# Kernel optimization log

Hardware: AMD Instinct MI355X
Metric: run time of the kernel (lower is better)

## Reference

```python
import jax, jax.numpy as jnp
import numpy as np


def setup_inputs() -> dict:
    key = jax.random.key(0)
    ks = jax.random.split(key, 8)
    B, C, H, W = 16, 512, 96, 96
    Cr = C // 8
    s = 0.02
    return {
        "x": jax.random.normal(ks[0], (B, C, H, W), jnp.float32),
        "Wq": jax.random.normal(ks[1], (Cr, C), jnp.float32) * s,
        "bq": jax.random.normal(ks[2], (Cr,), jnp.float32) * s,
        "Wk": jax.random.normal(ks[3], (Cr, C), jnp.float32) * s,
        "bk": jax.random.normal(ks[4], (Cr,), jnp.float32) * s,
        "Wv": jax.random.normal(ks[5], (C, C), jnp.float32) * s,
        "bv": jax.random.normal(ks[6], (C,), jnp.float32) * s,
        "gamma": jax.random.normal(ks[7], (1,), jnp.float32) * 0.1,
    }


def _conv1x1(x, W, b):
    # 1x1 conv == channel contraction: [B,C,H,W] x [O,C] -> [B,O,H,W]
    return jnp.einsum('bchw,oc->bohw', x, W) + b[None, :, None, None]


def reference(x, Wq, bq, Wk, bk, Wv, bv, gamma):
    B, C, H, W = x.shape
    q = _conv1x1(x, Wq, bq)   # [B,Cr,H,W]
    k = _conv1x1(x, Wk, bk)   # [B,Cr,H,W]
    v = _conv1x1(x, Wv, bv)   # [B,C,H,W]

    # energy along column (vertical): query at (i,w), keys at (j,w) -> [B,H,W,H]
    eh = jnp.einsum('bciw,bcjw->biwj', q, k)
    # energy along row (horizontal): query at (h,i), keys at (h,j) -> [B,H,W,W]
    ew = jnp.einsum('bchi,bchj->bhij', q, k)

    attn = jax.nn.softmax(jnp.concatenate([eh, ew], axis=-1), axis=-1)  # [B,H,W,H+W]
    ah = attn[..., :H]   # [B,H,W,H]
    aw = attn[..., H:]   # [B,H,W,W]

    out_h = jnp.einsum('bcjw,biwj->bciw', v, ah)  # vertical aggregation
    out_w = jnp.einsum('bchj,bhij->bchi', v, aw)  # horizontal aggregation
    out = out_h + out_w
    return gamma[0] * out + x
```

## Files before the change

kernel.cpp:

```cpp
#include <hip/hip_runtime.h>
#include <hip/hip_bf16.h>

#define DI __device__ __forceinline__

typedef short bf16x8 __attribute__((ext_vector_type(8)));
typedef float f32x4 __attribute__((ext_vector_type(4)));
typedef unsigned short u16;
typedef u16 u16x2 __attribute__((ext_vector_type(2)));
typedef u16 u16x8 __attribute__((ext_vector_type(8)));

#define B_ 16
#define C_ 512
#define CR_ 64
#define H_ 96
#define HW_ 9216
#define K_ 512

DI float b2f(u16 u){ unsigned v = ((unsigned)u)<<16; float f; __builtin_memcpy(&f,&v,4); return f; }
DI u16 f2b(float f){ unsigned v; __builtin_memcpy(&v,&f,4); v += 0x7fff + ((v>>16)&1); return (u16)(v>>16); }

DI void gload16(const void* g, void* l){
  __builtin_amdgcn_global_load_lds((const __attribute__((address_space(1))) unsigned*)g,
                                   (__attribute__((address_space(3))) unsigned*)l, 16, 0, 0);
}

__global__ __launch_bounds__(256) void k_pack(const float* __restrict__ Wq, const float* __restrict__ bq,
    const float* __restrict__ Wk, const float* __restrict__ bk,
    const float* __restrict__ Wv, const float* __restrict__ bv,
    u16* __restrict__ Wcat, float* __restrict__ bcat){
  int gid = blockIdx.x*256 + threadIdx.x;
  int o = gid >> 9, c = gid & 511;
  float w = (o < 64) ? Wq[o*512 + c] : (o < 128) ? Wk[(o-64)*512 + c] : Wv[(o-128)*512 + c];
  Wcat[gid] = f2b(w);
  if (c == 0) bcat[o] = (o < 64) ? bq[o] : (o < 128) ? bk[o-64] : bv[o-128];
}

__global__ __launch_bounds__(256) void k_xt(const float* __restrict__ x, u16* __restrict__ xt){
  int bx = blockIdx.x;
  int pt = bx % 144; int ct = (bx/144) & 7; int b = bx / (144*8);
  __shared__ u16 tile[64][68];
  int tx = threadIdx.x & 63, ty = threadIdx.x >> 6;
  const float* xb = x + (size_t)b*C_*HW_;
  for (int r = ty; r < 64; r += 4)
    tile[r][tx] = f2b(xb[(size_t)(ct*64 + r)*HW_ + pt*64 + tx]);
  __syncthreads();
  u16* xtb = xt + (size_t)b*HW_*K_;
  for (int r = ty; r < 64; r += 4)
    xtb[(size_t)(pt*64 + r)*K_ + ct*64 + tx] = tile[tx][r];
}

__global__ __launch_bounds__(256) void k_qkv(const u16* __restrict__ Wcat, const float* __restrict__ bcat,
    const u16* __restrict__ xt, u16* __restrict__ q, u16* __restrict__ k, u16* __restrict__ v){
  int bx = blockIdx.x;
  int wg = (bx & 7)*720 + (bx >> 3);
  int nt = wg % 72; int tmp = wg / 72; int mt = tmp % 5; int b = tmp / 5;
  __shared__ u16 As[128*64];
  __shared__ u16 Bs[128*64];
  int lane = threadIdx.x & 63, wid = threadIdx.x >> 6;
  int wr = wid >> 1, wc = wid & 1;
  const u16* xb = xt + (size_t)b*HW_*K_ + (size_t)nt*128*K_;
  const u16* Ab = Wcat + (size_t)mt*128*K_;

  f32x4 acc[4][4];
  #pragma unroll
  for (int i=0;i<4;++i)
    #pragma unroll
    for (int j=0;j<4;++j) acc[i][j] = (f32x4){0.f,0.f,0.f,0.f};

  int ibase = wid*4;
  for (int kt=0; kt<8; ++kt){
    int k0 = kt*64;
    __syncthreads();
    #pragma unroll
    for (int i=0;i<4;++i){
      int byteL = ((ibase + i)<<10) + (lane<<4);
      int row = byteL >> 7;
      int slog = ((byteL >> 4) & 7) ^ (row & 7);
      size_t ge = (size_t)row*K_ + (k0 + slog*8);
      gload16(Ab + ge, (char*)As + ((ibase+i)<<10));
      gload16(xb + ge, (char*)Bs + ((ibase+i)<<10));
    }
    __syncthreads();
    bf16x8 af[4][2], bfr[4][2];
    #pragma unroll
    for (int f=0; f<4; ++f){
      #pragma unroll
      for (int kk=0; kk<2; ++kk){
        int sl = kk*4 + (lane >> 4);
        int ra = wr*64 + f*16 + (lane & 15);
        af[f][kk]  = *(const bf16x8*)((const char*)As + ra*128 + ((sl ^ (ra & 7))<<4));
        int rb = wc*64 + f*16 + (lane & 15);
        bfr[f][kk] = *(const bf16x8*)((const char*)Bs + rb*128 + ((sl ^ (rb & 7))<<4));
      }
    }
    #pragma unroll
    for (int fm=0; fm<4; ++fm)
      #pragma unroll
      for (int fn=0; fn<4; ++fn)
        #pragma unroll
        for (int kk=0; kk<2; ++kk)
          acc[fm][fn] = __builtin_amdgcn_mfma_f32_16x16x32_bf16(af[fm][kk], bfr[fn][kk], acc[fm][fn], 0, 0, 0);
  }
  int r4 = lane >> 4, cl = lane & 15;
  for (int fm=0; fm<4; ++fm){
    for (int j=0;j<4;++j){
      int o = mt*128 + wr*64 + fm*16 + r4*4 + j;
      float bias = bcat[o];
      for (int fn=0; fn<4; ++fn){
        int n = nt*128 + wc*64 + fn*16 + cl;
        u16 bv16 = f2b(acc[fm][fn][j] + bias);
        if (o < 64)       q[((size_t)b*CR_ + o)*HW_ + n] = bv16;
        else if (o < 128) k[((size_t)b*CR_ + (o-64))*HW_ + n] = bv16;
        else              v[((size_t)b*C_ + (o-128))*HW_ + n] = bv16;
      }
    }
  }
}

__global__ __launch_bounds__(256) void k_tr(const u16* __restrict__ q, const u16* __restrict__ k,
    const u16* __restrict__ v, u16* __restrict__ qt, u16* __restrict__ kt, u16* __restrict__ vt){
  int bx = blockIdx.x;
  int ch = bx % 640; int b = bx / 640;
  const u16* src; u16* dst;
  if (ch < 64)      { src = q + ((size_t)b*CR_ + ch)*HW_;      dst = qt + ((size_t)b*CR_ + ch)*HW_; }
  else if (ch < 128){ src = k + ((size_t)b*CR_ + ch-64)*HW_;   dst = kt + ((size_t)b*CR_ + ch-64)*HW_; }
  else              { src = v + ((size_t)b*C_ + ch-128)*HW_;   dst = vt + ((size_t)b*C_ + ch-128)*HW_; }
  __shared__ u16 t[96][100];
  for (int e = threadIdx.x; e < HW_; e += 256) t[e/96][e%96] = src[e];
  __syncthreads();
  for (int e = threadIdx.x; e < HW_; e += 256) dst[e] = t[e%96][e/96];
}

__global__ __launch_bounds__(256) void k_scores(const u16* __restrict__ q, const u16* __restrict__ k,
    const u16* __restrict__ qt, const u16* __restrict__ kt, u16* __restrict__ att){
  int bx = blockIdx.x;
  int p = bx % 96; int b = (bx/96) & 15; int mode = bx / 1536;
  __shared__ float Qs[64*96];
  __shared__ float Ks[64*96];
  const u16* qsrc; const u16* ksrc;
  if (mode == 0){ qsrc = qt + (size_t)b*CR_*HW_ + p*96; ksrc = kt + (size_t)b*CR_*HW_ + p*96; }
  else          { qsrc = q  + (size_t)b*CR_*HW_ + p*96; ksrc = k  + (size_t)b*CR_*HW_ + p*96; }
  for (int u = threadIdx.x; u < 64*12; u += 256){
    int c = u / 12, ch = u % 12;
    u16x8 a = *(const u16x8*)(qsrc + (size_t)c*HW_ + ch*8);
    u16x8 d = *(const u16x8*)(ksrc + (size_t)c*HW_ + ch*8);
    #pragma unroll
    for (int e=0;e<8;++e){ Qs[c*96 + ch*8 + e] = b2f(a[e]); Ks[c*96 + ch*8 + e] = b2f(d[e]); }
  }
  __syncthreads();
  int ti = threadIdx.x >> 4, tj = threadIdx.x & 15;
  float acc[6][6];
  #pragma unroll
  for (int a2=0;a2<6;++a2)
    #pragma unroll
    for (int b2=0;b2<6;++b2) acc[a2][b2] = 0.f;
  for (int c=0;c<64;++c){
    float qv[6], kv[6];
    #pragma unroll
    for (int a2=0;a2<6;++a2){ qv[a2] = Qs[c*96 + ti + 16*a2]; kv[a2] = Ks[c*96 + tj + 16*a2]; }
    #pragma unroll
    for (int a2=0;a2<6;++a2)
      #pragma unroll
      for (int b2=0;b2<6;++b2) acc[a2][b2] += qv[a2]*kv[b2];
  }
  for (int a2=0;a2<6;++a2){
    int i = ti + 16*a2;
    for (int b2=0;b2<6;++b2){
      int j = tj + 16*b2;
      size_t idx = (mode==0) ? ((size_t)((b*96 + i)*96 + p))*192 + j
                             : ((size_t)((b*96 + p)*96 + i))*192 + 96 + j;
      att[idx] = f2b(acc[a2][b2]);
    }
  }
}

__global__ __launch_bounds__(256) void k_softmax(u16* __restrict__ att){
  int row = blockIdx.x*4 + (threadIdx.x >> 6);
  int lane = threadIdx.x & 63;
  u16* r = att + (size_t)row*192;
  float s0 = b2f(r[lane]), s1 = b2f(r[lane+64]), s2 = b2f(r[lane+128]);
  float m = fmaxf(fmaxf(s0,s1),s2);
  #pragma unroll
  for (int off=32; off; off>>=1) m = fmaxf(m, __shfl_xor(m, off));
  float e0 = expf(s0-m), e1 = expf(s1-m), e2 = expf(s2-m);
  float s = e0+e1+e2;
  #pragma unroll
  for (int off=32; off; off>>=1) s += __shfl_xor(s, off);
  float inv = 1.0f/s;
  r[lane] = f2b(e0*inv); r[lane+64] = f2b(e1*inv); r[lane+128] = f2b(e2*inv);
}

__global__ __launch_bounds__(512) void k_outh(const u16* __restrict__ vt, const u16* __restrict__ att,
    u16* __restrict__ oh){
  int bx = blockIdx.x; int w = bx % 96, b = bx / 96;
  __shared__ u16 Ah[96*104];
  for (int u = threadIdx.x; u < 96*48; u += 512){
    int i = u/48, jc = u%48;
    *(u16x2*)&Ah[i*104 + jc*2] = *(const u16x2*)(att + ((size_t)((b*96 + i)*96 + w))*192 + jc*2);
  }
  __syncthreads();
  int lane = threadIdx.x & 63, wid = threadIdx.x >> 6;
  int cl = lane & 15, r4 = lane >> 4;
  f32x4 acc[4][6];
  #pragma unroll
  for (int i=0;i<4;++i)
    #pragma unroll
    for (int j=0;j<6;++j) acc[i][j] = (f32x4){0.f,0.f,0.f,0.f};
  const u16* vb = vt + (size_t)b*C_*HW_ + (size_t)w*96;
  #pragma unroll
  for (int kt=0; kt<3; ++kt){
    int kof = kt*32 + r4*8;
    bf16x8 a[4], bb[6];
    #pragma unroll
    for (int fm=0; fm<4; ++fm){
      int c = wid*64 + fm*16 + cl;
      a[fm] = *(const bf16x8*)(vb + (size_t)c*HW_ + kof);
    }
    #pragma unroll
    for (int fn=0; fn<6; ++fn)
      bb[fn] = *(const bf16x8*)&Ah[(fn*16 + cl)*104 + kof];
    #pragma unroll
    for (int fm=0; fm<4; ++fm)
      #pragma unroll
      for (int fn=0; fn<6; ++fn)
        acc[fm][fn] = __builtin_amdgcn_mfma_f32_16x16x32_bf16(a[fm], bb[fn], acc[fm][fn], 0, 0, 0);
  }
  u16* ob = oh + ((size_t)(b*96 + w))*C_*96;
  for (int fm=0; fm<4; ++fm)
    for (int fn=0; fn<6; ++fn)
      for (int j=0;j<4;++j){
        int c = wid*64 + fm*16 + r4*4 + j;
        int i = fn*16 + cl;
        ob[(size_t)c*96 + i] = f2b(acc[fm][fn][j]);
      }
}

__global__ __launch_bounds__(512) void k_outw(const u16* __restrict__ v, const u16* __restrict__ att,
    const float* __restrict__ gp, float* __restrict__ out){
  int bx = blockIdx.x; int h = bx % 96, b = bx / 96;
  __shared__ u16 Aw[96*104];
  for (int u = threadIdx.x; u < 96*48; u += 512){
    int i = u/48, jc = u%48;
    *(u16x2*)&Aw[i*104 + jc*2] = *(const u16x2*)(att + ((size_t)((b*96 + h)*96 + i))*192 + 96 + jc*2);
  }
  __syncthreads();
  float g = gp[0];
  int lane = threadIdx.x & 63, wid = threadIdx.x >> 6;
  int cl = lane & 15, r4 = lane >> 4;
  f32x4 acc[4][6];
  #pragma unroll
  for (int i=0;i<4;++i)
    #pragma unroll
    for (int j=0;j<6;++j) acc[i][j] = (f32x4){0.f,0.f,0.f,0.f};
  const u16* vb = v + (size_t)b*C_*HW_ + (size_t)h*96;
  #pragma unroll
  for (int kt=0; kt<3; ++kt){
    int kof = kt*32 + r4*8;
    bf16x8 a[4], bb[6];
    #pragma unroll
    for (int fm=0; fm<4; ++fm){
      int c = wid*64 + fm*16 + cl;
      a[fm] = *(const bf16x8*)(vb + (size_t)c*HW_ + kof);
    }
    #pragma unroll
    for (int fn=0; fn<6; ++fn)
      bb[fn] = *(const bf16x8*)&Aw[(fn*16 + cl)*104 + kof];
    #pragma unroll
    for (int fm=0; fm<4; ++fm)
      #pragma unroll
      for (int fn=0; fn<6; ++fn)
        acc[fm][fn] = __builtin_amdgcn_mfma_f32_16x16x32_bf16(a[fm], bb[fn], acc[fm][fn], 0, 0, 0);
  }
  float* ob = out + (size_t)b*C_*HW_ + (size_t)h*96;
  for (int fm=0; fm<4; ++fm)
    for (int fn=0; fn<6; ++fn)
      for (int j=0;j<4;++j){
        int c = wid*64 + fm*16 + r4*4 + j;
        int i = fn*16 + cl;
        ob[(size_t)c*HW_ + i] = g * acc[fm][fn][j];
      }
}

__global__ __launch_bounds__(256) void k_final(const u16* __restrict__ oh, const float* __restrict__ x,
    const float* __restrict__ gp, float* __restrict__ out){
  int bx = blockIdx.x; int c = bx & 511; int b = bx >> 9;
  __shared__ u16 T[96*104];
  const u16* ohb = oh + (size_t)(b*96)*C_*96 + (size_t)c*96;
  for (int e = threadIdx.x; e < HW_; e += 256){
    int w = e/96, i = e%96;
    T[w*104 + i] = ohb[(size_t)w*C_*96 + i];
  }
  __syncthreads();
  float g = gp[0];
  size_t base = ((size_t)b*C_ + c)*HW_;
  for (int e = threadIdx.x; e < HW_; e += 256){
    int i = e/96, w = e%96;
    out[base + e] = out[base + e] + g*b2f(T[w*104 + i]) + x[base + e];
  }
}

extern "C" void kernel_launch(void* const* d_in, const int* in_sizes, int n_in,
                              void* d_out, int out_size, void* d_ws, size_t ws_size,
                              hipStream_t stream) {
  (void)in_sizes; (void)n_in; (void)out_size; (void)ws_size;
  const float* x  = (const float*)d_in[0];
  const float* Wq = (const float*)d_in[1];
  const float* bq = (const float*)d_in[2];
  const float* Wk = (const float*)d_in[3];
  const float* bk = (const float*)d_in[4];
  const float* Wv = (const float*)d_in[5];
  const float* bv = (const float*)d_in[6];
  const float* gm = (const float*)d_in[7];
  float* out = (float*)d_out;
  char* ws = (char*)d_ws;

  u16*  Wcat = (u16*)(ws);
  float* bcat= (float*)(ws + 655360);
  u16*  q    = (u16*)(ws + 659456);
  u16*  k    = (u16*)(ws + 19533824);
  u16*  qt   = (u16*)(ws + 38408192);
  u16*  kt   = (u16*)(ws + 57282560);
  u16*  v    = (u16*)(ws + 76156928);
  u16*  att  = (u16*)(ws + 227151872);
  u16*  oh   = (u16*)(ws + 283774976);
  u16*  xt   = (u16*)d_out;
  u16*  vt   = xt + 75497472ull;

  k_pack   <<<1280, 256, 0, stream>>>(Wq,bq,Wk,bk,Wv,bv,Wcat,bcat);
  k_xt     <<<18432,256, 0, stream>>>(x, xt);
  k_qkv    <<<5760, 256, 0, stream>>>(Wcat,bcat,xt,q,k,v);
  k_tr     <<<10240,256, 0, stream>>>(q,k,v,qt,kt,vt);
  k_scores <<<3072, 256, 0, stream>>>(q,k,qt,kt,att);
  k_softmax<<<36864,256, 0, stream>>>(att);
  k_outh   <<<1536, 512, 0, stream>>>(vt,att,oh);
  k_outw   <<<1536, 512, 0, stream>>>(v,att,gm,out);
  k_final  <<<8192, 256, 0, stream>>>(oh,x,gm,out);
}
```

Before: 890.5 us.

## Vectorize transposes, write bf16 outputs in place, and fuse final epilogue

Rewrites the x and q/k/v transposes to use 16-byte vector loads and stores through XOR-swizzled shared memory. Softmax now handles rows with 32 lanes and fast exp. The two aggregation kernels write bf16 results in place over their V inputs, replacing the fp32 out write and the separate oh buffer. The final kernel then reads both bf16 partials with vector accesses and applies gamma and the residual. This reduces global traffic, especially the fp32 read-modify-write of out, at the cost of bf16 rounding of the horizontal partial and in-place overwrites that depend on each block reading its full V slice before writing.

Result: faster. 824.6 us (-7.4%).

```diff
diff --git a/kernel.cpp b/kernel.cpp
--- a/kernel.cpp
+++ b/kernel.cpp
@@ -7,6 +7,7 @@
 typedef float f32x4 __attribute__((ext_vector_type(4)));
 typedef unsigned short u16;
 typedef u16 u16x2 __attribute__((ext_vector_type(2)));
+typedef u16 u16x4 __attribute__((ext_vector_type(4)));
 typedef u16 u16x8 __attribute__((ext_vector_type(8)));
 
 #define B_ 16
@@ -38,15 +39,23 @@
 __global__ __launch_bounds__(256) void k_xt(const float* __restrict__ x, u16* __restrict__ xt){
   int bx = blockIdx.x;
   int pt = bx % 144; int ct = (bx/144) & 7; int b = bx / (144*8);
-  __shared__ u16 tile[64][68];
-  int tx = threadIdx.x & 63, ty = threadIdx.x >> 6;
-  const float* xb = x + (size_t)b*C_*HW_;
-  for (int r = ty; r < 64; r += 4)
-    tile[r][tx] = f2b(xb[(size_t)(ct*64 + r)*HW_ + pt*64 + tx]);
-  __syncthreads();
-  u16* xtb = xt + (size_t)b*HW_*K_;
-  for (int r = ty; r < 64; r += 4)
-    xtb[(size_t)(pt*64 + r)*K_ + ct*64 + tx] = tile[tx][r];
+  __shared__ u16 T[64*72];
+  const float* xb = x + (size_t)b*C_*HW_ + (size_t)(ct*64)*HW_ + pt*64;
+  for (int it = threadIdx.x; it < 1024; it += 256){
+    int r = it & 63, px4 = it >> 6;
+    f32x4 f4 = *(const f32x4*)(xb + (size_t)r*HW_ + px4*4);
+    #pragma unroll
+    for (int e=0;e<4;++e) T[(px4*4 + e)*72 + r] = f2b(f4[e]);
+  }
+  __syncthreads();
+  u16* xtb = xt + (size_t)b*HW_*K_ + (size_t)(pt*64)*K_ + ct*64;
+  for (int it = threadIdx.x; it < 512; it += 256){
+    int c8 = it & 7, p = it >> 3;
+    u16x8 o;
+    #pragma unroll
+    for (int e=0;e<8;++e) o[e] = T[p*72 + c8*8 + e];
+    *(u16x8*)(xtb + (size_t)p*K_ + c8*8) = o;
+  }
 }
 
 __global__ __launch_bounds__(256) void k_qkv(const u16* __restrict__ Wcat, const float* __restrict__ bcat,
@@ -117,18 +126,32 @@
   }
 }
 
-__global__ __launch_bounds__(256) void k_tr(const u16* __restrict__ q, const u16* __restrict__ k,
+__global__ __launch_bounds__(256) void k_tr(const u16* __restrict__ q, const u16* __restrict__ kk,
     const u16* __restrict__ v, u16* __restrict__ qt, u16* __restrict__ kt, u16* __restrict__ vt){
   int bx = blockIdx.x;
   int ch = bx % 640; int b = bx / 640;
   const u16* src; u16* dst;
-  if (ch < 64)      { src = q + ((size_t)b*CR_ + ch)*HW_;      dst = qt + ((size_t)b*CR_ + ch)*HW_; }
-  else if (ch < 128){ src = k + ((size_t)b*CR_ + ch-64)*HW_;   dst = kt + ((size_t)b*CR_ + ch-64)*HW_; }
-  else              { src = v + ((size_t)b*C_ + ch-128)*HW_;   dst = vt + ((size_t)b*C_ + ch-128)*HW_; }
-  __shared__ u16 t[96][100];
-  for (int e = threadIdx.x; e < HW_; e += 256) t[e/96][e%96] = src[e];
-  __syncthreads();
-  for (int e = threadIdx.x; e < HW_; e += 256) dst[e] = t[e%96][e/96];
+  if (ch < 64)      { src = q  + ((size_t)b*CR_ + ch)*HW_;     dst = qt + ((size_t)b*CR_ + ch)*HW_; }
+  else if (ch < 128){ src = kk + ((size_t)b*CR_ + ch-64)*HW_;  dst = kt + ((size_t)b*CR_ + ch-64)*HW_; }
+  else              { src = v  + ((size_t)b*C_ + ch-128)*HW_;  dst = vt + ((size_t)b*C_ + ch-128)*HW_; }
+  __shared__ u16 T[96*128];
+  for (int it = threadIdx.x; it < 1152; it += 256){
+    int h = it / 12, c8 = it % 12;
+    u16x8 v8 = *(const u16x8*)(src + h*96 + c8*8);
+    int sp = (h >> 3) ^ (c8 & 7);
+    #pragma unroll
+    for (int e = 0; e < 8; ++e){
+      int w = c8*8 + e;
+      T[w*128 + sp*8 + (h & 7)] = v8[e];
+    }
+  }
+  __syncthreads();
+  for (int it = threadIdx.x; it < 1152; it += 256){
+    int w = it / 12, h8 = it % 12;
+    int sp = h8 ^ ((w >> 3) & 7);
+    u16x8 o = *(const u16x8*)&T[w*128 + sp*8];
+    *(u16x8*)(dst + (size_t)w*96 + h8*8) = o;
+  }
 }
 
 __global__ __launch_bounds__(256) void k_scores(const u16* __restrict__ q, const u16* __restrict__ k,
@@ -175,23 +198,24 @@
 }
 
 __global__ __launch_bounds__(256) void k_softmax(u16* __restrict__ att){
-  int row = blockIdx.x*4 + (threadIdx.x >> 6);
-  int lane = threadIdx.x & 63;
-  u16* r = att + (size_t)row*192;
-  float s0 = b2f(r[lane]), s1 = b2f(r[lane+64]), s2 = b2f(r[lane+128]);
-  float m = fmaxf(fmaxf(s0,s1),s2);
-  #pragma unroll
-  for (int off=32; off; off>>=1) m = fmaxf(m, __shfl_xor(m, off));
-  float e0 = expf(s0-m), e1 = expf(s1-m), e2 = expf(s2-m);
-  float s = e0+e1+e2;
-  #pragma unroll
-  for (int off=32; off; off>>=1) s += __shfl_xor(s, off);
+  int row = blockIdx.x*8 + (threadIdx.x >> 5);
+  int sub = threadIdx.x & 31;
+  u16* r = att + (size_t)row*192 + sub*6;
+  u16x2 a = *(u16x2*)r, b = *(u16x2*)(r+2), c = *(u16x2*)(r+4);
+  float v0=b2f(a[0]),v1=b2f(a[1]),v2=b2f(b[0]),v3=b2f(b[1]),v4=b2f(c[0]),v5=b2f(c[1]);
+  float m = fmaxf(fmaxf(fmaxf(v0,v1),fmaxf(v2,v3)),fmaxf(v4,v5));
+  #pragma unroll
+  for (int off=16; off; off>>=1) m = fmaxf(m, __shfl_xor(m, off));
+  float e0=__expf(v0-m),e1=__expf(v1-m),e2=__expf(v2-m),e3=__expf(v3-m),e4=__expf(v4-m),e5=__expf(v5-m);
+  float s = ((e0+e1)+(e2+e3))+(e4+e5);
+  #pragma unroll
+  for (int off=16; off; off>>=1) s += __shfl_xor(s, off);
   float inv = 1.0f/s;
-  r[lane] = f2b(e0*inv); r[lane+64] = f2b(e1*inv); r[lane+128] = f2b(e2*inv);
-}
-
-__global__ __launch_bounds__(512) void k_outh(const u16* __restrict__ vt, const u16* __restrict__ att,
-    u16* __restrict__ oh){
+  a[0]=f2b(e0*inv); a[1]=f2b(e1*inv); b[0]=f2b(e2*inv); b[1]=f2b(e3*inv); c[0]=f2b(e4*inv); c[1]=f2b(e5*inv);
+  *(u16x2*)r = a; *(u16x2*)(r+2) = b; *(u16x2*)(r+4) = c;
+}
+
+__global__ __launch_bounds__(512) void k_outh(u16* vo, const u16* __restrict__ att){
   int bx = blockIdx.x; int w = bx % 96, b = bx / 96;
   __shared__ u16 Ah[96*104];
   for (int u = threadIdx.x; u < 96*48; u += 512){
@@ -206,7 +230,7 @@
   for (int i=0;i<4;++i)
     #pragma unroll
     for (int j=0;j<6;++j) acc[i][j] = (f32x4){0.f,0.f,0.f,0.f};
-  const u16* vb = vt + (size_t)b*C_*HW_ + (size_t)w*96;
+  u16* vb = vo + (size_t)b*C_*HW_ + (size_t)w*96;
   #pragma unroll
   for (int kt=0; kt<3; ++kt){
     int kof = kt*32 + r4*8;
@@ -225,18 +249,16 @@
       for (int fn=0; fn<6; ++fn)
         acc[fm][fn] = __builtin_amdgcn_mfma_f32_16x16x32_bf16(a[fm], bb[fn], acc[fm][fn], 0, 0, 0);
   }
-  u16* ob = oh + ((size_t)(b*96 + w))*C_*96;
   for (int fm=0; fm<4; ++fm)
     for (int fn=0; fn<6; ++fn)
       for (int j=0;j<4;++j){
         int c = wid*64 + fm*16 + r4*4 + j;
         int i = fn*16 + cl;
-        ob[(size_t)c*96 + i] = f2b(acc[fm][fn][j]);
+        vb[(size_t)c*HW_ + i] = f2b(acc[fm][fn][j]);
       }
 }
 
-__global__ __launch_bounds__(512) void k_outw(const u16* __restrict__ v, const u16* __restrict__ att,
-    const float* __restrict__ gp, float* __restrict__ out){
+__global__ __launch_bounds__(512) void k_outw(u16* vo, const u16* __restrict__ att){
   int bx = blockIdx.x; int h = bx % 96, b = bx / 96;
   __shared__ u16 Aw[96*104];
   for (int u = threadIdx.x; u < 96*48; u += 512){
@@ -244,7 +266,6 @@
     *(u16x2*)&Aw[i*104 + jc*2] = *(const u16x2*)(att + ((size_t)((b*96 + h)*96 + i))*192 + 96 + jc*2);
   }
   __syncthreads();
-  float g = gp[0];
   int lane = threadIdx.x & 63, wid = threadIdx.x >> 6;
   int cl = lane & 15, r4 = lane >> 4;
   f32x4 acc[4][6];
@@ -252,7 +273,7 @@
   for (int i=0;i<4;++i)
     #pragma unroll
     for (int j=0;j<6;++j) acc[i][j] = (f32x4){0.f,0.f,0.f,0.f};
-  const u16* vb = v + (size_t)b*C_*HW_ + (size_t)h*96;
+  u16* vb = vo + (size_t)b*C_*HW_ + (size_t)h*96;
   #pragma unroll
   for (int kt=0; kt<3; ++kt){
     int kof = kt*32 + r4*8;
@@ -271,31 +292,44 @@
       for (int fn=0; fn<6; ++fn)
         acc[fm][fn] = __builtin_amdgcn_mfma_f32_16x16x32_bf16(a[fm], bb[fn], acc[fm][fn], 0, 0, 0);
   }
-  float* ob = out + (size_t)b*C_*HW_ + (size_t)h*96;
   for (int fm=0; fm<4; ++fm)
     for (int fn=0; fn<6; ++fn)
       for (int j=0;j<4;++j){
         int c = wid*64 + fm*16 + r4*4 + j;
         int i = fn*16 + cl;
-        ob[(size_t)c*HW_ + i] = g * acc[fm][fn][j];
+        vb[(size_t)c*HW_ + i] = f2b(acc[fm][fn][j]);
       }
 }
 
-__global__ __launch_bounds__(256) void k_final(const u16* __restrict__ oh, const float* __restrict__ x,
-    const float* __restrict__ gp, float* __restrict__ out){
+__global__ __launch_bounds__(256) void k_final(const u16* oh, const u16* ow,
+    const float* __restrict__ x, const float* __restrict__ gp, float* __restrict__ out){
   int bx = blockIdx.x; int c = bx & 511; int b = bx >> 9;
-  __shared__ u16 T[96*104];
-  const u16* ohb = oh + (size_t)(b*96)*C_*96 + (size_t)c*96;
-  for (int e = threadIdx.x; e < HW_; e += 256){
-    int w = e/96, i = e%96;
-    T[w*104 + i] = ohb[(size_t)w*C_*96 + i];
+  size_t base = ((size_t)b*C_ + c)*HW_;
+  const u16* ohc = oh + base;
+  const u16* owc = ow + base;
+  __shared__ u16 T[96*128];
+  for (int it = threadIdx.x; it < 1152; it += 256){
+    int w = it / 12, c8 = it % 12;
+    u16x8 v8 = *(const u16x8*)(ohc + w*96 + c8*8);
+    int sp = (w >> 3) ^ (c8 & 7);
+    #pragma unroll
+    for (int e = 0; e < 8; ++e){
+      int i = c8*8 + e;
+      T[i*128 + sp*8 + (w & 7)] = v8[e];
+    }
   }
   __syncthreads();
   float g = gp[0];
-  size_t base = ((size_t)b*C_ + c)*HW_;
-  for (int e = threadIdx.x; e < HW_; e += 256){
-    int i = e/96, w = e%96;
-    out[base + e] = out[base + e] + g*b2f(T[w*104 + i]) + x[base + e];
+  for (int it = threadIdx.x; it < 2304; it += 256){
+    int i = it / 24, w4 = it % 24; int w = w4*4;
+    int sp = (w >> 3) ^ ((i >> 3) & 7);
+    u16x4 t4 = *(const u16x4*)&T[i*128 + sp*8 + (w & 7)];
+    u16x4 o4 = *(const u16x4*)(owc + i*96 + w);
+    f32x4 x4 = *(const f32x4*)(x + base + i*96 + w);
+    f32x4 r;
+    #pragma unroll
+    for (int e=0;e<4;++e) r[e] = g*(b2f(t4[e]) + b2f(o4[e])) + x4[e];
+    *(f32x4*)(out + base + i*96 + w) = r;
   }
 }
 
@@ -322,17 +356,16 @@
   u16*  kt   = (u16*)(ws + 57282560);
   u16*  v    = (u16*)(ws + 76156928);
   u16*  att  = (u16*)(ws + 227151872);
-  u16*  oh   = (u16*)(ws + 283774976);
+  u16*  vt   = (u16*)(ws + 283774976);
   u16*  xt   = (u16*)d_out;
-  u16*  vt   = xt + 75497472ull;
 
   k_pack   <<<1280, 256, 0, stream>>>(Wq,bq,Wk,bk,Wv,bv,Wcat,bcat);
   k_xt     <<<18432,256, 0, stream>>>(x, xt);
   k_qkv    <<<5760, 256, 0, stream>>>(Wcat,bcat,xt,q,k,v);
   k_tr     <<<10240,256, 0, stream>>>(q,k,v,qt,kt,vt);
   k_scores <<<3072, 256, 0, stream>>>(q,k,qt,kt,att);
-  k_softmax<<<36864,256, 0, stream>>>(att);
-  k_outh   <<<1536, 512, 0, stream>>>(vt,att,oh);
-  k_outw   <<<1536, 512, 0, stream>>>(v,att,gm,out);
-  k_final  <<<8192, 256, 0, stream>>>(oh,x,gm,out);
-}
+  k_softmax<<<18432,256, 0, stream>>>(att);
+  k_outh   <<<1536, 512, 0, stream>>>(vt,att);
+  k_outw   <<<1536, 512, 0, stream>>>(v,att);
+  k_final  <<<8192, 256, 0, stream>>>(vt,v,x,gm,out);
+}
```
